# Performance work log

Hardware: AMD Instinct MI355X
Metric: run time of the kernel (lower is better)

The kernel has to match this reference:

```python
import jax, jax.numpy as jnp
import numpy as np

T, N, F_IN = 5, 10000, 16
E = 160000
C = 32          # gat_hidden_dim (per head)
H0 = 2          # heads in layer 0 (concat) -> out 64
GRU = 64
OUT_H = 32


def setup_inputs() -> dict:
    key = jax.random.key(0)
    ks = jax.random.split(key, 24)
    s = 0.1
    inp = {
        "x_seq": jax.random.normal(ks[0], (T, N, F_IN), jnp.float32),
        "edge_index": jax.random.randint(ks[1], (2, E), 0, N, jnp.int32),
        # GAT layer 0: in 16 -> 2 heads x 32, concat -> 64
        "gat0_W": s * jax.random.normal(ks[2], (F_IN, H0 * C), jnp.float32),
        "gat0_asrc": s * jax.random.normal(ks[3], (H0, C), jnp.float32),
        "gat0_adst": s * jax.random.normal(ks[4], (H0, C), jnp.float32),
        "gat0_b": s * jax.random.normal(ks[5], (H0 * C,), jnp.float32),
        "res0_W": s * jax.random.normal(ks[6], (F_IN, H0 * C), jnp.float32),   # [in,out]
        # GAT layer 1: in 64 -> 1 head x 32, no concat -> 32
        "gat1_W": s * jax.random.normal(ks[7], (H0 * C, C), jnp.float32),
        "gat1_asrc": s * jax.random.normal(ks[8], (1, C), jnp.float32),
        "gat1_adst": s * jax.random.normal(ks[9], (1, C), jnp.float32),
        "gat1_b": s * jax.random.normal(ks[10], (C,), jnp.float32),
        "res1_W": s * jax.random.normal(ks[11], (H0 * C, C), jnp.float32),
        # GRU cells (torch GRUCell layout: W_i [3H,in], W_h [3H,H])
        "gru0_Wi": s * jax.random.normal(ks[12], (3 * GRU, C), jnp.float32),
        "gru0_Wh": s * jax.random.normal(ks[13], (3 * GRU, GRU), jnp.float32),
        "gru0_bi": s * jax.random.normal(ks[14], (3 * GRU,), jnp.float32),
        "gru0_bh": s * jax.random.normal(ks[15], (3 * GRU,), jnp.float32),
        "gru1_Wi": s * jax.random.normal(ks[16], (3 * GRU, GRU), jnp.float32),
        "gru1_Wh": s * jax.random.normal(ks[17], (3 * GRU, GRU), jnp.float32),
        "gru1_bi": s * jax.random.normal(ks[18], (3 * GRU,), jnp.float32),
        "gru1_bh": s * jax.random.normal(ks[19], (3 * GRU,), jnp.float32),
        # MLP head
        "fc1_W": s * jax.random.normal(ks[20], (GRU, OUT_H), jnp.float32),
        "fc1_b": s * jax.random.normal(ks[21], (OUT_H,), jnp.float32),
        "fc2_W": s * jax.random.normal(ks[22], (OUT_H, 1), jnp.float32),
        "fc2_b": s * jax.random.normal(ks[23], (1,), jnp.float32),
    }
    return inp


def _gat(x, src, dst, n, W, a_src, a_dst, b, heads, concat):
    ch = W.shape[1] // heads
    xw = (x @ W).reshape(n, heads, ch)                      # [N,H,C]
    al_s = (xw * a_src).sum(-1)                             # [N,H]
    al_d = (xw * a_dst).sum(-1)
    e = jax.nn.leaky_relu(al_s[src] + al_d[dst], 0.2)       # [Etot,H]
    m = jax.ops.segment_max(e, dst, num_segments=n)
    ex = jnp.exp(e - m[dst])
    den = jax.ops.segment_sum(ex, dst, num_segments=n)
    alpha = ex / (den[dst] + 1e-16)                         # scatter-softmax
    out = jax.ops.segment_sum(alpha[:, :, None] * xw[src], dst, num_segments=n)
    out = out.reshape(n, heads * ch) if concat else out.mean(axis=1)
    return out + b


def _gru(x, h, Wi, Wh, bi, bh):
    gi = x @ Wi.T + bi
    gh = h @ Wh.T + bh
    i_r, i_z, i_n = jnp.split(gi, 3, axis=-1)
    h_r, h_z, h_n = jnp.split(gh, 3, axis=-1)
    r = jax.nn.sigmoid(i_r + h_r)
    z = jax.nn.sigmoid(i_z + h_z)
    nn_ = jnp.tanh(i_n + r * h_n)
    return (1.0 - z) * nn_ + z * h


def reference(x_seq, edge_index,
              gat0_W, gat0_asrc, gat0_adst, gat0_b, res0_W,
              gat1_W, gat1_asrc, gat1_adst, gat1_b, res1_W,
              gru0_Wi, gru0_Wh, gru0_bi, gru0_bh,
              gru1_Wi, gru1_Wh, gru1_bi, gru1_bh,
              fc1_W, fc1_b, fc2_W, fc2_b):
    n = x_seq.shape[1]
    loops = jnp.arange(n, dtype=edge_index.dtype)
    src = jnp.concatenate([edge_index[0], loops])           # PyG adds self-loops
    dst = jnp.concatenate([edge_index[1], loops])

    def step(carry, x_t):
        h0, h1 = carry
        x1 = jax.nn.elu(_gat(x_t, src, dst, n, gat0_W, gat0_asrc, gat0_adst, gat0_b, 2, True)) + x_t @ res0_W
        x2 = jax.nn.elu(_gat(x1, src, dst, n, gat1_W, gat1_asrc, gat1_adst, gat1_b, 1, False)) + x1 @ res1_W
        h0 = _gru(x2, h0, gru0_Wi, gru0_Wh, gru0_bi, gru0_bh)
        h1 = _gru(h0, h1, gru1_Wi, gru1_Wh, gru1_bi, gru1_bh)
        return (h0, h1), None

    h0 = jnp.zeros((n, gru0_Wh.shape[1]), x_seq.dtype)
    h1 = jnp.zeros((n, gru1_Wh.shape[1]), x_seq.dtype)
    (h0, h1), _ = jax.lax.scan(step, (h0, h1), x_seq)
    h = jax.nn.relu(h1 @ fc1_W + fc1_b)
    return h @ fc2_W + fc2_b                                # [N,1]
```

## Files before the change

kernel.cpp:

```cpp
#include <hip/hip_runtime.h>
#include <hip/hip_bf16.h>
#include <math.h>

#define T_STEPS 5
#define NNODES  10000
#define NM      (T_STEPS * NNODES)
#define F_IN    16
#define NEDGES  160000
#define ETOT    (NEDGES + NNODES)
#define GW      8
#define GNPW    5

#define RL(v, k) __int_as_float(__builtin_amdgcn_readlane(__float_as_int(v), (k)))

__global__ __launch_bounds__(256) void k_count(const int* __restrict__ ei, int* __restrict__ counts) {
    int idx = blockIdx.x * 256 + threadIdx.x;
    if (idx >= ETOT) return;
    int dst = (idx < NEDGES) ? ei[NEDGES + idx] : (idx - NEDGES);
    atomicAdd(&counts[dst], 1);
}

__global__ __launch_bounds__(1024) void k_scan(const int* __restrict__ counts, int* __restrict__ offs) {
    __shared__ int ssum[1024];
    int t = threadIdx.x;
    const int chunk = (NNODES + 1023) / 1024;
    int start = t * chunk, end = min(start + chunk, NNODES);
    int s = 0;
    for (int i = start; i < end; i++) s += counts[i];
    ssum[t] = s;
    __syncthreads();
    for (int off = 1; off < 1024; off <<= 1) {
        int v = (t >= off) ? ssum[t - off] : 0;
        __syncthreads();
        ssum[t] += v;
        __syncthreads();
    }
    int excl = (t == 0) ? 0 : ssum[t - 1];
    for (int i = start; i < end; i++) { offs[i] = excl; excl += counts[i]; }
    if (t == 1023) offs[NNODES] = ssum[1023];
}

__global__ __launch_bounds__(256) void k_fill(const int* __restrict__ ei, const int* __restrict__ offs,
                                              int* __restrict__ cursor, int* __restrict__ csr) {
    int idx = blockIdx.x * 256 + threadIdx.x;
    if (idx >= ETOT) return;
    int src, dst;
    if (idx < NEDGES) { src = ei[idx]; dst = ei[NEDGES + idx]; }
    else              { src = dst = idx - NEDGES; }
    int p = atomicAdd(&cursor[dst], 1);
    csr[offs[dst] + p] = src;
}

__global__ __launch_bounds__(256) void k_transpose(const float* __restrict__ Wi0, const float* __restrict__ Wh0,
                                                   const float* __restrict__ Wi1, const float* __restrict__ Wh1,
                                                   float* __restrict__ WiT0, float* __restrict__ WhT0,
                                                   float* __restrict__ WiT1, float* __restrict__ WhT1) {
    int idx = blockIdx.x * 256 + threadIdx.x;
    if (idx < 32 * 192) {
        int k = idx / 192, r = idx % 192;
        WiT0[idx] = Wi0[r * 32 + k];
        return;
    }
    idx -= 32 * 192;
    if (idx < 64 * 192) {
        int k = idx / 192, r = idx % 192;
        WhT0[idx] = Wh0[r * 64 + k];
        return;
    }
    idx -= 64 * 192;
    if (idx < 64 * 192) {
        int k = idx / 192, r = idx % 192;
        WiT1[idx] = Wi1[r * 64 + k];
        return;
    }
    idx -= 64 * 192;
    if (idx < 64 * 192) {
        int k = idx / 192, r = idx % 192;
        WhT1[idx] = Wh1[r * 64 + k];
    }
}

__global__ __launch_bounds__(256) void k_mm0_all(const float* __restrict__ x,
                                                 const float* __restrict__ W,
                                                 const float* __restrict__ Wres,
                                                 const float* __restrict__ asrc,
                                                 const float* __restrict__ adst,
                                                 float* __restrict__ xw, float* __restrict__ xres,
                                                 float* __restrict__ als, float* __restrict__ ald) {
    int wave = threadIdx.x >> 6, lane = threadIdx.x & 63;
    int m = blockIdx.x * 4 + wave;
    if (m >= NM) return;
    const float* xr = x + (size_t)m * F_IN;
    float xreg[F_IN];
#pragma unroll
    for (int k = 0; k < F_IN; k++) xreg[k] = xr[k];
    float acc = 0.f, accr = 0.f;
#pragma unroll
    for (int k = 0; k < F_IN; k++) {
        acc  += xreg[k] * W[k * 64 + lane];
        accr += xreg[k] * Wres[k * 64 + lane];
    }
    xw[(size_t)m * 64 + lane]   = acc;
    xres[(size_t)m * 64 + lane] = accr;
    float ps = acc * asrc[lane], pd = acc * adst[lane];
    for (int off = 16; off; off >>= 1) {
        ps += __shfl_down(ps, off, 32);
        pd += __shfl_down(pd, off, 32);
    }
    if ((lane & 31) == 0) {
        int h = lane >> 5;
        als[m * 2 + h] = ps;
        ald[m * 2 + h] = pd;
    }
}

__global__ __launch_bounds__(256) void k_gat0_all(const float* __restrict__ xw,
                                                  const float* __restrict__ xres,
                                                  const float* __restrict__ als,
                                                  const float* __restrict__ ald,
                                                  const int* __restrict__ offs, const int* __restrict__ csr,
                                                  const float* __restrict__ b,
                                                  const float* __restrict__ W1,
                                                  const float* __restrict__ Wres1,
                                                  const float* __restrict__ as1,
                                                  const float* __restrict__ ad1v,
                                                  float* __restrict__ xw1, float* __restrict__ xres1,
                                                  float* __restrict__ als1, float* __restrict__ ald1) {
    int wave = threadIdx.x >> 6, lane = threadIdx.x & 63;
    int m = blockIdx.x * 4 + wave;
    if (m >= NM) return;
    int t = m / NNODES;
    int node = m - t * NNODES;
    int base = t * NNODES;
    int beg = offs[node], end = offs[node + 1];
    int deg = end - beg;
    float ad0 = ald[m * 2 + 0], ad1 = ald[m * 2 + 1];
    float acc;
    if (deg <= 64) {
        int s = 0; float e0 = -INFINITY, e1 = -INFINITY;
        if (lane < deg) {
            s = base + csr[beg + lane];
            e0 = als[s * 2 + 0] + ad0; e0 = e0 > 0.f ? e0 : 0.2f * e0;
            e1 = als[s * 2 + 1] + ad1; e1 = e1 > 0.f ? e1 : 0.2f * e1;
        }
        float m0 = e0, m1 = e1;
        for (int o = 32; o; o >>= 1) {
            m0 = fmaxf(m0, __shfl_xor(m0, o));
            m1 = fmaxf(m1, __shfl_xor(m1, o));
        }
        float ex0 = (lane < deg) ? expf(e0 - m0) : 0.f;
        float ex1 = (lane < deg) ? expf(e1 - m1) : 0.f;
        float d0 = ex0, d1 = ex1;
        for (int o = 32; o; o >>= 1) {
            d0 += __shfl_xor(d0, o);
            d1 += __shfl_xor(d1, o);
        }
        ex0 *= 1.f / (d0 + 1e-16f);
        ex1 *= 1.f / (d1 + 1e-16f);
        float a0 = 0.f, a1 = 0.f, a2 = 0.f, a3 = 0.f;
        int i = 0;
        for (; i + 4 <= deg; i += 4) {
            int   s0 = __shfl(s, i),     s1 = __shfl(s, i + 1), s2 = __shfl(s, i + 2), s3 = __shfl(s, i + 3);
            float u0 = __shfl(ex0, i),   v0 = __shfl(ex1, i);
            float u1 = __shfl(ex0, i+1), v1 = __shfl(ex1, i+1);
            float u2 = __shfl(ex0, i+2), v2 = __shfl(ex1, i+2);
            float u3 = __shfl(ex0, i+3), v3 = __shfl(ex1, i+3);
            a0 += (lane < 32 ? u0 : v0) * xw[(size_t)s0 * 64 + lane];
            a1 += (lane < 32 ? u1 : v1) * xw[(size_t)s1 * 64 + lane];
            a2 += (lane < 32 ? u2 : v2) * xw[(size_t)s2 * 64 + lane];
            a3 += (lane < 32 ? u3 : v3) * xw[(size_t)s3 * 64 + lane];
        }
        for (; i < deg; i++) {
            int s0 = __shfl(s, i);
            float u = __shfl(ex0, i), v = __shfl(ex1, i);
            a0 += (lane < 32 ? u : v) * xw[(size_t)s0 * 64 + lane];
        }
        acc = (a0 + a1) + (a2 + a3);
    } else {
        float m0 = -INFINITY, m1 = -INFINITY;
        for (int i = beg + lane; i < end; i += 64) {
            int s = base + csr[i];
            float e0 = als[s * 2 + 0] + ad0; e0 = e0 > 0.f ? e0 : 0.2f * e0;
            float e1 = als[s * 2 + 1] + ad1; e1 = e1 > 0.f ? e1 : 0.2f * e1;
            m0 = fmaxf(m0, e0); m1 = fmaxf(m1, e1);
        }
        for (int o = 32; o; o >>= 1) {
            m0 = fmaxf(m0, __shfl_xor(m0, o));
            m1 = fmaxf(m1, __shfl_xor(m1, o));
        }
        float d0 = 0.f, d1 = 0.f;
        for (int i = beg + lane; i < end; i += 64) {
            int s = base + csr[i];
            float e0 = als[s * 2 + 0] + ad0; e0 = e0 > 0.f ? e0 : 0.2f * e0;
            float e1 = als[s * 2 + 1] + ad1; e1 = e1 > 0.f ? e1 : 0.2f * e1;
            d0 += expf(e0 - m0); d1 += expf(e1 - m1);
        }
        for (int o = 32; o; o >>= 1) { d0 += __shfl_xor(d0, o); d1 += __shfl_xor(d1, o); }
        float inv0 = 1.f / (d0 + 1e-16f), inv1 = 1.f / (d1 + 1e-16f);
        acc = 0.f;
        for (int i = beg; i < end; i++) {
            int s = base + csr[i];
            float e, wgt;
            if (lane < 32) { e = als[s * 2 + 0] + ad0; e = e > 0.f ? e : 0.2f * e; wgt = expf(e - m0) * inv0; }
            else           { e = als[s * 2 + 1] + ad1; e = e > 0.f ? e : 0.2f * e; wgt = expf(e - m1) * inv1; }
            acc += wgt * xw[(size_t)s * 64 + lane];
        }
    }
    float x1v = acc + b[lane];
    x1v = x1v > 0.f ? x1v : expm1f(x1v);
    x1v += xres[(size_t)m * 64 + lane];
    int j = lane & 31;
    const float* Wp = (lane < 32) ? W1 : Wres1;
    float pacc = 0.f;
#pragma unroll
    for (int k = 0; k < 64; k++) {
        float xv = RL(x1v, k);
        pacc += xv * Wp[k * 32 + j];
    }
    if (lane < 32) xw1[(size_t)m * 32 + j]   = pacc;
    else           xres1[(size_t)m * 32 + j] = pacc;
    float ps = (lane < 32) ? pacc * as1[j]  : 0.f;
    float pd = (lane < 32) ? pacc * ad1v[j] : 0.f;
    for (int o = 16; o; o >>= 1) {
        ps += __shfl_down(ps, o, 32);
        pd += __shfl_down(pd, o, 32);
    }
    if (lane == 0) { als1[m] = ps; ald1[m] = pd; }
}

__global__ __launch_bounds__(256) void k_gat1_all(const float* __restrict__ xw1,
                                                  const float* __restrict__ xres1,
                                                  const float* __restrict__ als1,
                                                  const float* __restrict__ ald1,
                                                  const int* __restrict__ offs, const int* __restrict__ csr,
                                                  const float* __restrict__ b,
                                                  float* __restrict__ x2) {
    int wave = threadIdx.x >> 6, lane = threadIdx.x & 63;
    int m = blockIdx.x * 4 + wave;
    if (m >= NM) return;
    int t = m / NNODES;
    int node = m - t * NNODES;
    int base = t * NNODES;
    int beg = offs[node], end = offs[node + 1];
    int deg = end - beg;
    float adv = ald1[m];
    int ch = lane & 31, half = lane >> 5;
    float aggr;
    if (deg <= 64) {
        int s = 0; float e = -INFINITY;
        if (lane < deg) {
            s = base + csr[beg + lane];
            e = als1[s] + adv; e = e > 0.f ? e : 0.2f * e;
        }
        float mx = e;
        for (int o = 32; o; o >>= 1) mx = fmaxf(mx, __shfl_xor(mx, o));
        float ex = (lane < deg) ? expf(e - mx) : 0.f;
        float d = ex;
        for (int o = 32; o; o >>= 1) d += __shfl_xor(d, o);
        ex *= 1.f / (d + 1e-16f);
        float acc = 0.f;
        for (int i = 0; i < deg; i += 2) {
            int i2 = (i + 1 < deg) ? i + 1 : i;
            int   sa = __shfl(s, i),  sb = __shfl(s, i2);
            float wa = __shfl(ex, i), wb = __shfl(ex, i2);
            if (i + 1 >= deg) wb = 0.f;
            int   sm = half ? sb : sa;
            float wm = half ? wb : wa;
            acc += wm * xw1[(size_t)sm * 32 + ch];
        }
        acc += __shfl_xor(acc, 32);
        aggr = acc;
    } else {
        float mx = -INFINITY;
        for (int i = beg + lane; i < end; i += 64) {
            float e = als1[base + csr[i]] + adv; e = e > 0.f ? e : 0.2f * e;
            mx = fmaxf(mx, e);
        }
        for (int o = 32; o; o >>= 1) mx = fmaxf(mx, __shfl_xor(mx, o));
        float d = 0.f;
        for (int i = beg + lane; i < end; i += 64) {
            float e = als1[base + csr[i]] + adv; e = e > 0.f ? e : 0.2f * e;
            d += expf(e - mx);
        }
        for (int o = 32; o; o >>= 1) d += __shfl_xor(d, o);
        float inv = 1.f / (d + 1e-16f);
        float acc = 0.f;
        for (int i = beg; i < end; i++) {
            int s = base + csr[i];
            float e = als1[s] + adv; e = e > 0.f ? e : 0.2f * e;
            float wgt = expf(e - mx) * inv;
            acc += wgt * xw1[(size_t)s * 32 + ch];
        }
        aggr = acc;
    }
    if (lane < 32) {
        float v = aggr + b[ch];
        v = v > 0.f ? v : expm1f(v);
        x2[(size_t)m * 32 + ch] = v + xres1[(size_t)m * 32 + ch];
    }
}

__global__ __launch_bounds__(512) void k_gruhead(const float* __restrict__ x2,
                                                 const float* __restrict__ WiT0,
                                                 const float* __restrict__ WhT0,
                                                 const float* __restrict__ WiT1,
                                                 const float* __restrict__ WhT1,
                                                 const float* __restrict__ bi0, const float* __restrict__ bh0,
                                                 const float* __restrict__ bi1, const float* __restrict__ bh1,
                                                 const float* __restrict__ fc1W,
                                                 const float* __restrict__ fc1b,
                                                 const float* __restrict__ fc2W,
                                                 const float* __restrict__ fc2b,
                                                 float* __restrict__ out) {
    __shared__ float lw[64 * 192];
    int tid = threadIdx.x;
    int wave = tid >> 6, lane = tid & 63;
    int node0 = (blockIdx.x * GW + wave) * GNPW;

    float bir0 = bi0[lane] + bh0[lane];
    float biz0 = bi0[64 + lane] + bh0[64 + lane];
    float bin0 = bi0[128 + lane], bhn0 = bh0[128 + lane];
    float bir1 = bi1[lane] + bh1[lane];
    float biz1 = bi1[64 + lane] + bh1[64 + lane];
    float bin1 = bi1[128 + lane], bhn1 = bh1[128 + lane];

    float h0[GNPW] = {0.f, 0.f, 0.f, 0.f, 0.f};
    float h1[GNPW] = {0.f, 0.f, 0.f, 0.f, 0.f};

    auto stage = [&](const float* __restrict__ src) {
        __syncthreads();
        const float4* s4 = (const float4*)src;
        float4* d4 = (float4*)lw;
#pragma unroll
        for (int i = 0; i < 6; i++) d4[tid + i * 512] = s4[tid + i * 512];
        __syncthreads();
    };

    for (int t = 0; t < T_STEPS; t++) {
        size_t rb = ((size_t)t * NNODES + node0) * 32;
        float xa = x2[rb + lane];
        float xb = x2[rb + 64 + lane];
        float xc = x2[rb + 128 + (lane & 31)];

        float gr[GNPW], gz[GNPW], gin[GNPW], ghn[GNPW];
#pragma unroll
        for (int n = 0; n < GNPW; n++) { gr[n] = bir0; gz[n] = biz0; gin[n] = bin0; ghn[n] = bhn0; }
#pragma unroll 4
        for (int k = 0; k < 32; k++) {
            float wr = WiT0[k * 192 + lane];
            float wz = WiT0[k * 192 + 64 + lane];
            float wn = WiT0[k * 192 + 128 + lane];
            float xv[GNPW];
            xv[0] = RL(xa, k); xv[1] = RL(xa, 32 + k);
            xv[2] = RL(xb, k); xv[3] = RL(xb, 32 + k);
            xv[4] = RL(xc, k);
#pragma unroll
            for (int n = 0; n < GNPW; n++) {
                gr[n] += xv[n] * wr; gz[n] += xv[n] * wz; gin[n] += xv[n] * wn;
            }
        }
        stage(WhT0);
#pragma unroll 4
        for (int k = 0; k < 64; k++) {
            float wr = lw[k * 192 + lane];
            float wz = lw[k * 192 + 64 + lane];
            float wn = lw[k * 192 + 128 + lane];
#pragma unroll
            for (int n = 0; n < GNPW; n++) {
                float hv = RL(h0[n], k);
                gr[n] += hv * wr; gz[n] += hv * wz; ghn[n] += hv * wn;
            }
        }
#pragma unroll
        for (int n = 0; n < GNPW; n++) {
            float r = 1.f / (1.f + expf(-gr[n]));
            float z = 1.f / (1.f + expf(-gz[n]));
            float nn = tanhf(gin[n] + r * ghn[n]);
            h0[n] = (1.f - z) * nn + z * h0[n];
        }

#pragma unroll
        for (int n = 0; n < GNPW; n++) { gr[n] = bir1; gz[n] = biz1; gin[n] = bin1; }
        stage(WiT1);
#pragma unroll 4
        for (int k = 0; k < 64; k++) {
            float wir = lw[k * 192 + lane];
            float wiz = lw[k * 192 + 64 + lane];
            float win = lw[k * 192 + 128 + lane];
#pragma unroll
            for (int n = 0; n < GNPW; n++) {
                float xv = RL(h0[n], k);
                gr[n] += xv * wir; gz[n] += xv * wiz; gin[n] += xv * win;
            }
        }
#pragma unroll
        for (int n = 0; n < GNPW; n++) ghn[n] = bhn1;
        stage(WhT1);
#pragma unroll 4
        for (int k = 0; k < 64; k++) {
            float whr = lw[k * 192 + lane];
            float whz = lw[k * 192 + 64 + lane];
            float whn = lw[k * 192 + 128 + lane];
#pragma unroll
            for (int n = 0; n < GNPW; n++) {
                float hv = RL(h1[n], k);
                gr[n] += hv * whr; gz[n] += hv * whz; ghn[n] += hv * whn;
            }
        }
#pragma unroll
        for (int n = 0; n < GNPW; n++) {
            float r = 1.f / (1.f + expf(-gr[n]));
            float z = 1.f / (1.f + expf(-gz[n]));
            float nn = tanhf(gin[n] + r * ghn[n]);
            h1[n] = (1.f - z) * nn + z * h1[n];
        }
    }

    int j = lane & 31, half = lane >> 5;
#pragma unroll
    for (int p = 0; p < 3; p++) {
        int ne = 2 * p;
        int no = (2 * p + 1 < GNPW) ? 2 * p + 1 : 2 * p;
        float a = fc1b[j];
#pragma unroll
        for (int k = 0; k < 64; k++) {
            float he = RL(h1[ne], k);
            float ho = RL(h1[no], k);
            a += (half ? ho : he) * fc1W[k * 32 + j];
        }
        a = fmaxf(a, 0.f);
        float v = a * fc2W[j];
        for (int o = 16; o; o >>= 1) v += __shfl_down(v, o, 32);
        if ((lane & 31) == 0 && 2 * p + half < GNPW) out[node0 + 2 * p + half] = v + fc2b[0];
    }
}

extern "C" void kernel_launch(void* const* d_in, const int* in_sizes, int n_in,
                              void* d_out, int out_size, void* d_ws, size_t ws_size,
                              hipStream_t stream) {
    const float* x_seq   = (const float*)d_in[0];
    const int*   ei      = (const int*)d_in[1];
    const float* gat0_W  = (const float*)d_in[2];
    const float* gat0_as = (const float*)d_in[3];
    const float* gat0_ad = (const float*)d_in[4];
    const float* gat0_b  = (const float*)d_in[5];
    const float* res0_W  = (const float*)d_in[6];
    const float* gat1_W  = (const float*)d_in[7];
    const float* gat1_as = (const float*)d_in[8];
    const float* gat1_ad = (const float*)d_in[9];
    const float* gat1_b  = (const float*)d_in[10];
    const float* res1_W  = (const float*)d_in[11];
    const float* gru0_Wi = (const float*)d_in[12];
    const float* gru0_Wh = (const float*)d_in[13];
    const float* gru0_bi = (const float*)d_in[14];
    const float* gru0_bh = (const float*)d_in[15];
    const float* gru1_Wi = (const float*)d_in[16];
    const float* gru1_Wh = (const float*)d_in[17];
    const float* gru1_bi = (const float*)d_in[18];
    const float* gru1_bh = (const float*)d_in[19];
    const float* fc1_W   = (const float*)d_in[20];
    const float* fc1_b   = (const float*)d_in[21];
    const float* fc2_W   = (const float*)d_in[22];
    const float* fc2_b   = (const float*)d_in[23];
    float* out = (float*)d_out;

    char* w = (char*)d_ws;
    size_t off = 0;
    auto take = [&](size_t bytes) { size_t r = off; off += (bytes + 255) & ~(size_t)255; return r; };
    const size_t N = NNODES, M = NM;
    int*   counts = (int*)(w + take(N * 4));
    int*   cursor = (int*)(w + take(N * 4));
    int*   offs   = (int*)(w + take((N + 1) * 4));
    int*   csr    = (int*)(w + take((size_t)ETOT * 4));
    float* xw0    = (float*)(w + take(M * 64 * 4));
    float* xres0  = (float*)(w + take(M * 64 * 4));
    float* als0   = (float*)(w + take(M * 2 * 4));
    float* ald0   = (float*)(w + take(M * 2 * 4));
    float* xw1    = (float*)(w + take(M * 32 * 4));
    float* xres1  = (float*)(w + take(M * 32 * 4));
    float* als1   = (float*)(w + take(M * 4));
    float* ald1   = (float*)(w + take(M * 4));
    float* x2     = (float*)(w + take(M * 32 * 4));
    float* wiT0   = (float*)(w + take(32 * 192 * 4));
    float* whT0   = (float*)(w + take(64 * 192 * 4));
    float* wiT1   = (float*)(w + take(64 * 192 * 4));
    float* whT1   = (float*)(w + take(64 * 192 * 4));

    hipMemsetAsync(counts, 0, N * 4, stream);
    hipMemsetAsync(cursor, 0, N * 4, stream);
    const int egrid = (ETOT + 255) / 256;
    k_count<<<egrid, 256, 0, stream>>>(ei, counts);
    k_scan<<<1, 1024, 0, stream>>>(counts, offs);
    k_fill<<<egrid, 256, 0, stream>>>(ei, offs, cursor, csr);
    const int ttot = 32 * 192 + 3 * 64 * 192;
    k_transpose<<<(ttot + 255) / 256, 256, 0, stream>>>(gru0_Wi, gru0_Wh, gru1_Wi, gru1_Wh,
                                                        wiT0, whT0, wiT1, whT1);

    const int mgrid = (NM + 3) / 4;
    k_mm0_all<<<mgrid, 256, 0, stream>>>(x_seq, gat0_W, res0_W, gat0_as, gat0_ad, xw0, xres0, als0, ald0);
    k_gat0_all<<<mgrid, 256, 0, stream>>>(xw0, xres0, als0, ald0, offs, csr, gat0_b,
                                          gat1_W, res1_W, gat1_as, gat1_ad,
                                          xw1, xres1, als1, ald1);
    k_gat1_all<<<mgrid, 256, 0, stream>>>(xw1, xres1, als1, ald1, offs, csr, gat1_b, x2);

    const int ggrid = NNODES / (GW * GNPW);
    k_gruhead<<<ggrid, 512, 0, stream>>>(x2, wiT0, whT0, wiT1, whT1,
                                         gru0_bi, gru0_bh, gru1_bi, gru1_bh,
                                         fc1_W, fc1_b, fc2_W, fc2_b, out);
}
```

Before: 382.2 us.

## Keep all GRU hidden weights resident in LDS with float4-packed layout

Adds a new GRU+head kernel that loads the three 64-wide GRU weight matrices once into 144KB of dynamic LDS, packed as float4 per output column, instead of restaging one matrix per gate pass. The input weights of the first GRU are read from global memory as float4. expf is replaced by __expf in the attention softmax and the GRU sigmoids. It relies on the device allowing 144KB of LDS per block and falls back to the old kernel otherwise, at the cost of one block per CU and slightly lower exp accuracy.

```diff
diff --git a/kernel.cpp b/kernel.cpp
--- a/kernel.cpp
+++ b/kernel.cpp
@@ -54,30 +54,29 @@
 __global__ __launch_bounds__(256) void k_transpose(const float* __restrict__ Wi0, const float* __restrict__ Wh0,
                                                    const float* __restrict__ Wi1, const float* __restrict__ Wh1,
                                                    float* __restrict__ WiT0, float* __restrict__ WhT0,
-                                                   float* __restrict__ WiT1, float* __restrict__ WhT1) {
+                                                   float* __restrict__ WiT1, float* __restrict__ WhT1,
+                                                   float4* __restrict__ wp0, float4* __restrict__ hp0,
+                                                   float4* __restrict__ ip1, float4* __restrict__ hp1) {
     int idx = blockIdx.x * 256 + threadIdx.x;
-    if (idx < 32 * 192) {
-        int k = idx / 192, r = idx % 192;
-        WiT0[idx] = Wi0[r * 32 + k];
-        return;
-    }
-    idx -= 32 * 192;
-    if (idx < 64 * 192) {
-        int k = idx / 192, r = idx % 192;
-        WhT0[idx] = Wh0[r * 64 + k];
-        return;
-    }
-    idx -= 64 * 192;
-    if (idx < 64 * 192) {
-        int k = idx / 192, r = idx % 192;
-        WiT1[idx] = Wi1[r * 64 + k];
-        return;
-    }
-    idx -= 64 * 192;
-    if (idx < 64 * 192) {
-        int k = idx / 192, r = idx % 192;
-        WhT1[idx] = Wh1[r * 64 + k];
-    }
+    if (idx < 6144)  { int k = idx / 192, r = idx % 192; WiT0[idx] = Wi0[r * 32 + k]; return; }
+    idx -= 6144;
+    if (idx < 12288) { int k = idx / 192, r = idx % 192; WhT0[idx] = Wh0[r * 64 + k]; return; }
+    idx -= 12288;
+    if (idx < 12288) { int k = idx / 192, r = idx % 192; WiT1[idx] = Wi1[r * 64 + k]; return; }
+    idx -= 12288;
+    if (idx < 12288) { int k = idx / 192, r = idx % 192; WhT1[idx] = Wh1[r * 64 + k]; return; }
+    idx -= 12288;
+    if (idx < 1536) { int k4 = idx / 192, c = idx % 192; const float* s = Wi0 + c * 32 + 4 * k4;
+                      wp0[idx] = make_float4(s[0], s[1], s[2], s[3]); return; }
+    idx -= 1536;
+    if (idx < 3072) { int k4 = idx / 192, c = idx % 192; const float* s = Wh0 + c * 64 + 4 * k4;
+                      hp0[idx] = make_float4(s[0], s[1], s[2], s[3]); return; }
+    idx -= 3072;
+    if (idx < 3072) { int k4 = idx / 192, c = idx % 192; const float* s = Wi1 + c * 64 + 4 * k4;
+                      ip1[idx] = make_float4(s[0], s[1], s[2], s[3]); return; }
+    idx -= 3072;
+    if (idx < 3072) { int k4 = idx / 192, c = idx % 192; const float* s = Wh1 + c * 64 + 4 * k4;
+                      hp1[idx] = make_float4(s[0], s[1], s[2], s[3]); }
 }
 
 __global__ __launch_bounds__(256) void k_mm0_all(const float* __restrict__ x,
@@ -148,8 +147,8 @@
             m0 = fmaxf(m0, __shfl_xor(m0, o));
             m1 = fmaxf(m1, __shfl_xor(m1, o));
         }
-        float ex0 = (lane < deg) ? expf(e0 - m0) : 0.f;
-        float ex1 = (lane < deg) ? expf(e1 - m1) : 0.f;
+        float ex0 = (lane < deg) ? __expf(e0 - m0) : 0.f;
+        float ex1 = (lane < deg) ? __expf(e1 - m1) : 0.f;
         float d0 = ex0, d1 = ex1;
         for (int o = 32; o; o >>= 1) {
             d0 += __shfl_xor(d0, o);
@@ -193,7 +192,7 @@
             int s = base + csr[i];
             float e0 = als[s * 2 + 0] + ad0; e0 = e0 > 0.f ? e0 : 0.2f * e0;
             float e1 = als[s * 2 + 1] + ad1; e1 = e1 > 0.f ? e1 : 0.2f * e1;
-            d0 += expf(e0 - m0); d1 += expf(e1 - m1);
+            d0 += __expf(e0 - m0); d1 += __expf(e1 - m1);
         }
         for (int o = 32; o; o >>= 1) { d0 += __shfl_xor(d0, o); d1 += __shfl_xor(d1, o); }
         float inv0 = 1.f / (d0 + 1e-16f), inv1 = 1.f / (d1 + 1e-16f);
@@ -201,8 +200,8 @@
         for (int i = beg; i < end; i++) {
             int s = base + csr[i];
             float e, wgt;
-            if (lane < 32) { e = als[s * 2 + 0] + ad0; e = e > 0.f ? e : 0.2f * e; wgt = expf(e - m0) * inv0; }
-            else           { e = als[s * 2 + 1] + ad1; e = e > 0.f ? e : 0.2f * e; wgt = expf(e - m1) * inv1; }
+            if (lane < 32) { e = als[s * 2 + 0] + ad0; e = e > 0.f ? e : 0.2f * e; wgt = __expf(e - m0) * inv0; }
+            else           { e = als[s * 2 + 1] + ad1; e = e > 0.f ? e : 0.2f * e; wgt = __expf(e - m1) * inv1; }
             acc += wgt * xw[(size_t)s * 64 + lane];
         }
     }
@@ -254,7 +253,7 @@
         }
         float mx = e;
         for (int o = 32; o; o >>= 1) mx = fmaxf(mx, __shfl_xor(mx, o));
-        float ex = (lane < deg) ? expf(e - mx) : 0.f;
+        float ex = (lane < deg) ? __expf(e - mx) : 0.f;
         float d = ex;
         for (int o = 32; o; o >>= 1) d += __shfl_xor(d, o);
         ex *= 1.f / (d + 1e-16f);
@@ -280,7 +279,7 @@
         float d = 0.f;
         for (int i = beg + lane; i < end; i += 64) {
             float e = als1[base + csr[i]] + adv; e = e > 0.f ? e : 0.2f * e;
-            d += expf(e - mx);
+            d += __expf(e - mx);
         }
         for (int o = 32; o; o >>= 1) d += __shfl_xor(d, o);
         float inv = 1.f / (d + 1e-16f);
@@ -288,7 +287,7 @@
         for (int i = beg; i < end; i++) {
             int s = base + csr[i];
             float e = als1[s] + adv; e = e > 0.f ? e : 0.2f * e;
-            float wgt = expf(e - mx) * inv;
+            float wgt = __expf(e - mx) * inv;
             acc += wgt * xw1[(size_t)s * 32 + ch];
         }
         aggr = acc;
@@ -297,6 +296,146 @@
         float v = aggr + b[ch];
         v = v > 0.f ? v : expm1f(v);
         x2[(size_t)m * 32 + ch] = v + xres1[(size_t)m * 32 + ch];
+    }
+}
+
+__global__ __launch_bounds__(512) void k_gruhead_p(const float* __restrict__ x2,
+                                                   const float4* __restrict__ wp0,
+                                                   const float4* __restrict__ hp0,
+                                                   const float4* __restrict__ ip1,
+                                                   const float4* __restrict__ hp1,
+                                                   const float* __restrict__ bi0, const float* __restrict__ bh0,
+                                                   const float* __restrict__ bi1, const float* __restrict__ bh1,
+                                                   const float* __restrict__ fc1W, const float* __restrict__ fc1b,
+                                                   const float* __restrict__ fc2W, const float* __restrict__ fc2b,
+                                                   float* __restrict__ out) {
+    extern __shared__ float4 lds4[];
+    float4* Lh0 = lds4;
+    float4* Li1 = lds4 + 3072;
+    float4* Lh1 = lds4 + 6144;
+    int tid = threadIdx.x, wave = tid >> 6, lane = tid & 63;
+    int node0 = (blockIdx.x * GW + wave) * GNPW;
+
+    for (int i = tid; i < 3072; i += 512) { Lh0[i] = hp0[i]; Li1[i] = ip1[i]; Lh1[i] = hp1[i]; }
+    __syncthreads();
+
+    float bir0 = bi0[lane] + bh0[lane];
+    float biz0 = bi0[64 + lane] + bh0[64 + lane];
+    float bin0 = bi0[128 + lane], bhn0 = bh0[128 + lane];
+    float bir1 = bi1[lane] + bh1[lane];
+    float biz1 = bi1[64 + lane] + bh1[64 + lane];
+    float bin1 = bi1[128 + lane], bhn1 = bh1[128 + lane];
+
+    float h0[GNPW] = {0.f, 0.f, 0.f, 0.f, 0.f};
+    float h1[GNPW] = {0.f, 0.f, 0.f, 0.f, 0.f};
+
+    for (int t = 0; t < T_STEPS; t++) {
+        size_t rb = ((size_t)t * NNODES + node0) * 32;
+        float xa = x2[rb + lane];
+        float xb = x2[rb + 64 + lane];
+        float xc = x2[rb + 128 + (lane & 31)];
+
+        float gr[GNPW], gz[GNPW], gin[GNPW], ghn[GNPW];
+#pragma unroll
+        for (int n = 0; n < GNPW; n++) { gr[n] = bir0; gz[n] = biz0; gin[n] = bin0; ghn[n] = bhn0; }
+#pragma unroll
+        for (int k4 = 0; k4 < 8; k4++) {
+            float4 wr = wp0[(k4 * 3 + 0) * 64 + lane];
+            float4 wz = wp0[(k4 * 3 + 1) * 64 + lane];
+            float4 wn = wp0[(k4 * 3 + 2) * 64 + lane];
+            int kb = 4 * k4;
+#pragma unroll
+            for (int n = 0; n < GNPW; n++) {
+                float x0, x1, x2v, x3;
+                if      (n == 0) { x0 = RL(xa, kb); x1 = RL(xa, kb+1); x2v = RL(xa, kb+2); x3 = RL(xa, kb+3); }
+                else if (n == 1) { x0 = RL(xa, 32+kb); x1 = RL(xa, 33+kb); x2v = RL(xa, 34+kb); x3 = RL(xa, 35+kb); }
+                else if (n == 2) { x0 = RL(xb, kb); x1 = RL(xb, kb+1); x2v = RL(xb, kb+2); x3 = RL(xb, kb+3); }
+                else if (n == 3) { x0 = RL(xb, 32+kb); x1 = RL(xb, 33+kb); x2v = RL(xb, 34+kb); x3 = RL(xb, 35+kb); }
+                else             { x0 = RL(xc, kb); x1 = RL(xc, kb+1); x2v = RL(xc, kb+2); x3 = RL(xc, kb+3); }
+                gr[n]  += x0 * wr.x + x1 * wr.y + x2v * wr.z + x3 * wr.w;
+                gz[n]  += x0 * wz.x + x1 * wz.y + x2v * wz.z + x3 * wz.w;
+                gin[n] += x0 * wn.x + x1 * wn.y + x2v * wn.z + x3 * wn.w;
+            }
+        }
+#pragma unroll 4
+        for (int k4 = 0; k4 < 16; k4++) {
+            float4 wr = Lh0[(k4 * 3 + 0) * 64 + lane];
+            float4 wz = Lh0[(k4 * 3 + 1) * 64 + lane];
+            float4 wn = Lh0[(k4 * 3 + 2) * 64 + lane];
+            int kb = 4 * k4;
+#pragma unroll
+            for (int n = 0; n < GNPW; n++) {
+                float x0 = RL(h0[n], kb), x1 = RL(h0[n], kb+1), x2v = RL(h0[n], kb+2), x3 = RL(h0[n], kb+3);
+                gr[n]  += x0 * wr.x + x1 * wr.y + x2v * wr.z + x3 * wr.w;
+                gz[n]  += x0 * wz.x + x1 * wz.y + x2v * wz.z + x3 * wz.w;
+                ghn[n] += x0 * wn.x + x1 * wn.y + x2v * wn.z + x3 * wn.w;
+            }
+        }
+#pragma unroll
+        for (int n = 0; n < GNPW; n++) {
+            float r = 1.f / (1.f + __expf(-gr[n]));
+            float z = 1.f / (1.f + __expf(-gz[n]));
+            float nn = tanhf(gin[n] + r * ghn[n]);
+            h0[n] = (1.f - z) * nn + z * h0[n];
+        }
+
+#pragma unroll
+        for (int n = 0; n < GNPW; n++) { gr[n] = bir1; gz[n] = biz1; gin[n] = bin1; }
+#pragma unroll 4
+        for (int k4 = 0; k4 < 16; k4++) {
+            float4 wr = Li1[(k4 * 3 + 0) * 64 + lane];
+            float4 wz = Li1[(k4 * 3 + 1) * 64 + lane];
+            float4 wn = Li1[(k4 * 3 + 2) * 64 + lane];
+            int kb = 4 * k4;
+#pragma unroll
+            for (int n = 0; n < GNPW; n++) {
+                float x0 = RL(h0[n], kb), x1 = RL(h0[n], kb+1), x2v = RL(h0[n], kb+2), x3 = RL(h0[n], kb+3);
+                gr[n]  += x0 * wr.x + x1 * wr.y + x2v * wr.z + x3 * wr.w;
+                gz[n]  += x0 * wz.x + x1 * wz.y + x2v * wz.z + x3 * wz.w;
+                gin[n] += x0 * wn.x + x1 * wn.y + x2v * wn.z + x3 * wn.w;
+            }
+        }
+#pragma unroll
+        for (int n = 0; n < GNPW; n++) ghn[n] = bhn1;
+#pragma unroll 4
+        for (int k4 = 0; k4 < 16; k4++) {
+            float4 wr = Lh1[(k4 * 3 + 0) * 64 + lane];
+            float4 wz = Lh1[(k4 * 3 + 1) * 64 + lane];
+            float4 wn = Lh1[(k4 * 3 + 2) * 64 + lane];
+            int kb = 4 * k4;
+#pragma unroll
+            for (int n = 0; n < GNPW; n++) {
+                float x0 = RL(h1[n], kb), x1 = RL(h1[n], kb+1), x2v = RL(h1[n], kb+2), x3 = RL(h1[n], kb+3);
+                gr[n]  += x0 * wr.x + x1 * wr.y + x2v * wr.z + x3 * wr.w;
+                gz[n]  += x0 * wz.x + x1 * wz.y + x2v * wz.z + x3 * wz.w;
+                ghn[n] += x0 * wn.x + x1 * wn.y + x2v * wn.z + x3 * wn.w;
+            }
+        }
+#pragma unroll
+        for (int n = 0; n < GNPW; n++) {
+            float r = 1.f / (1.f + __expf(-gr[n]));
+            float z = 1.f / (1.f + __expf(-gz[n]));
+            float nn = tanhf(gin[n] + r * ghn[n]);
+            h1[n] = (1.f - z) * nn + z * h1[n];
+        }
+    }
+
+    int j = lane & 31, half = lane >> 5;
+#pragma unroll
+    for (int p = 0; p < 3; p++) {
+        int ne = 2 * p;
+        int no = (2 * p + 1 < GNPW) ? 2 * p + 1 : 2 * p;
+        float a = fc1b[j];
+#pragma unroll
+        for (int k = 0; k < 64; k++) {
+            float he = RL(h1[ne], k);
+            float ho = RL(h1[no], k);
+            a += (half ? ho : he) * fc1W[k * 32 + j];
+        }
+        a = fmaxf(a, 0.f);
+        float v = a * fc2W[j];
+        for (int o = 16; o; o >>= 1) v += __shfl_down(v, o, 32);
+        if ((lane & 31) == 0 && 2 * p + half < GNPW) out[node0 + 2 * p + half] = v + fc2b[0];
     }
 }
 
@@ -307,10 +446,8 @@
                                                  const float* __restrict__ WhT1,
                                                  const float* __restrict__ bi0, const float* __restrict__ bh0,
                                                  const float* __restrict__ bi1, const float* __restrict__ bh1,
-                                                 const float* __restrict__ fc1W,
-                                                 const float* __restrict__ fc1b,
-                                                 const float* __restrict__ fc2W,
-                                                 const float* __restrict__ fc2b,
+                                                 const float* __restrict__ fc1W, const float* __restrict__ fc1b,
+                                                 const float* __restrict__ fc2W, const float* __restrict__ fc2b,
                                                  float* __restrict__ out) {
     __shared__ float lw[64 * 192];
     int tid = threadIdx.x;
@@ -373,12 +510,11 @@
         }
 #pragma unroll
         for (int n = 0; n < GNPW; n++) {
-            float r = 1.f / (1.f + expf(-gr[n]));
-            float z = 1.f / (1.f + expf(-gz[n]));
+            float r = 1.f / (1.f + __expf(-gr[n]));
+            float z = 1.f / (1.f + __expf(-gz[n]));
             float nn = tanhf(gin[n] + r * ghn[n]);
             h0[n] = (1.f - z) * nn + z * h0[n];
         }
-
 #pragma unroll
         for (int n = 0; n < GNPW; n++) { gr[n] = bir1; gz[n] = biz1; gin[n] = bin1; }
         stage(WiT1);
@@ -409,8 +545,8 @@
         }
 #pragma unroll
         for (int n = 0; n < GNPW; n++) {
-            float r = 1.f / (1.f + expf(-gr[n]));
-            float z = 1.f / (1.f + expf(-gz[n]));
+            float r = 1.f / (1.f + __expf(-gr[n]));
+            float z = 1.f / (1.f + __expf(-gz[n]));
             float nn = tanhf(gin[n] + r * ghn[n]);
             h1[n] = (1.f - z) * nn + z * h1[n];
         }
@@ -468,23 +604,27 @@
     size_t off = 0;
     auto take = [&](size_t bytes) { size_t r = off; off += (bytes + 255) & ~(size_t)255; return r; };
     const size_t N = NNODES, M = NM;
-    int*   counts = (int*)(w + take(N * 4));
-    int*   cursor = (int*)(w + take(N * 4));
-    int*   offs   = (int*)(w + take((N + 1) * 4));
-    int*   csr    = (int*)(w + take((size_t)ETOT * 4));
-    float* xw0    = (float*)(w + take(M * 64 * 4));
-    float* xres0  = (float*)(w + take(M * 64 * 4));
-    float* als0   = (float*)(w + take(M * 2 * 4));
-    float* ald0   = (float*)(w + take(M * 2 * 4));
-    float* xw1    = (float*)(w + take(M * 32 * 4));
-    float* xres1  = (float*)(w + take(M * 32 * 4));
-    float* als1   = (float*)(w + take(M * 4));
-    float* ald1   = (float*)(w + take(M * 4));
-    float* x2     = (float*)(w + take(M * 32 * 4));
-    float* wiT0   = (float*)(w + take(32 * 192 * 4));
-    float* whT0   = (float*)(w + take(64 * 192 * 4));
-    float* wiT1   = (float*)(w + take(64 * 192 * 4));
-    float* whT1   = (float*)(w + take(64 * 192 * 4));
+    int*    counts = (int*)(w + take(N * 4));
+    int*    cursor = (int*)(w + take(N * 4));
+    int*    offs   = (int*)(w + take((N + 1) * 4));
+    int*    csr    = (int*)(w + take((size_t)ETOT * 4));
+    float*  xw0    = (float*)(w + take(M * 64 * 4));
+    float*  xres0  = (float*)(w + take(M * 64 * 4));
+    float*  als0   = (float*)(w + take(M * 2 * 4));
+    float*  ald0   = (float*)(w + take(M * 2 * 4));
+    float*  xw1    = (float*)(w + take(M * 32 * 4));
+    float*  xres1  = (float*)(w + take(M * 32 * 4));
+    float*  als1   = (float*)(w + take(M * 4));
+    float*  ald1   = (float*)(w + take(M * 4));
+    float*  x2     = (float*)(w + take(M * 32 * 4));
+    float*  wiT0   = (float*)(w + take(32 * 192 * 4));
+    float*  whT0   = (float*)(w + take(64 * 192 * 4));
+    float*  wiT1   = (float*)(w + take(64 * 192 * 4));
+    float*  whT1   = (float*)(w + take(64 * 192 * 4));
+    float4* wp0    = (float4*)(w + take(1536 * 16));
+    float4* hp0    = (float4*)(w + take(3072 * 16));
+    float4* ip1    = (float4*)(w + take(3072 * 16));
+    float4* hp1    = (float4*)(w + take(3072 * 16));
 
     hipMemsetAsync(counts, 0, N * 4, stream);
     hipMemsetAsync(cursor, 0, N * 4, stream);
@@ -492,9 +632,10 @@
     k_count<<<egrid, 256, 0, stream>>>(ei, counts);
     k_scan<<<1, 1024, 0, stream>>>(counts, offs);
     k_fill<<<egrid, 256, 0, stream>>>(ei, offs, cursor, csr);
-    const int ttot = 32 * 192 + 3 * 64 * 192;
+    const int ttot = 6144 + 3 * 12288 + 1536 + 3 * 3072;
     k_transpose<<<(ttot + 255) / 256, 256, 0, stream>>>(gru0_Wi, gru0_Wh, gru1_Wi, gru1_Wh,
-                                                        wiT0, whT0, wiT1, whT1);
+                                                        wiT0, whT0, wiT1, whT1,
+                                                        wp0, hp0, ip1, hp1);
 
     const int mgrid = (NM + 3) / 4;
     k_mm0_all<<<mgrid, 256, 0, stream>>>(x_seq, gat0_W, res0_W, gat0_as, gat0_ad, xw0, xres0, als0, ald0);
@@ -504,7 +645,15 @@
     k_gat1_all<<<mgrid, 256, 0, stream>>>(xw1, xres1, als1, ald1, offs, csr, gat1_b, x2);
 
     const int ggrid = NNODES / (GW * GNPW);
-    k_gruhead<<<ggrid, 512, 0, stream>>>(x2, wiT0, whT0, wiT1, whT1,
-                                         gru0_bi, gru0_bh, gru1_bi, gru1_bh,
-                                         fc1_W, fc1_b, fc2_W, fc2_b, out);
-}
+    hipError_t ae = hipFuncSetAttribute(reinterpret_cast<const void*>(k_gruhead_p),
+                                        hipFuncAttributeMaxDynamicSharedMemorySize, 147456);
+    if (ae == hipSuccess) {
+        k_gruhead_p<<<ggrid, 512, 147456, stream>>>(x2, wp0, hp0, ip1, hp1,
+                                                    gru0_bi, gru0_bh, gru1_bi, gru1_bh,
+                                                    fc1_W, fc1_b, fc2_W, fc2_b, out);
+    } else {
+        k_gruhead<<<ggrid, 512, 0, stream>>>(x2, wiT0, whT0, wiT1, whT1,
+                                             gru0_bi, gru0_bh, gru1_bi, gru1_bh,
+                                             fc1_W, fc1_b, fc2_W, fc2_b, out);
+    }
+}
```

After: 380.7 us. No clear change (-0.4%).
